# Kernel optimization log

Hardware: AMD Instinct MI355X
Metric: run time of the kernel (lower is better)

The kernel has to match this reference:

```python
import jax, jax.numpy as jnp
import numpy as np

B, S, E, H = 4, 2048, 1024, 16
K = 9           # number of boundaries per batch (K-1 = 8 passages)
DH = E // H


def make_relevance_mask(boundaries, relevance_scores, seq_len):
    """Vectorized equivalent of the Python-loop mask builder.

    boundaries: (B, K) int, sorted; boundaries[:,0] == q_end.
    relevance_scores: (B, K-1) float.
    Returns float mask (B, S, S) with values {0, 1, relevance}.
    """
    Bsz, Kb = boundaries.shape
    idx = jnp.arange(seq_len, dtype=boundaries.dtype)
    # pid[b, s] = j s.t. boundaries[b, j] <= s < boundaries[b, j+1]; -1 before b[0]
    pid = jax.vmap(lambda bb: jnp.searchsorted(bb, idx, side='right'))(boundaries) - 1  # (B,S)
    in_pass = (pid >= 0) & (pid < Kb - 1)  # inside some passage span
    rel_g = jnp.take_along_axis(relevance_scores, jnp.clip(pid, 0, Kb - 2), axis=1)  # (B,S)
    # query rows (pos < q_end): columns in passage j -> relevance[j], else 1
    col_val = jnp.where(in_pass, rel_g, 1.0)  # (B,S)
    qrow = idx[None, :] < boundaries[:, :1]   # (B,S)
    # non-query rows: 1 iff same passage block, else 0
    same = in_pass[:, :, None] & in_pass[:, None, :] & (pid[:, :, None] == pid[:, None, :])
    mask = jnp.where(qrow[:, :, None], col_val[:, None, :], jnp.where(same, 1.0, 0.0))
    return mask.astype(jnp.float32)


def setup_inputs() -> dict:
    key = jax.random.key(0)
    k1, k2, k3, k4, k5, k6, k7 = jax.random.split(key, 7)
    hidden_states = jax.random.normal(k1, (B, S, E), dtype=jnp.float32)
    relevance_scores = jax.random.uniform(k2, (B, K - 1), dtype=jnp.float32)
    passage_boundaries = jnp.sort(jax.random.randint(k3, (B, K), 0, S, dtype=jnp.int32), axis=1)
    in_proj_w = 0.02 * jax.random.normal(k4, (3 * E, E), dtype=jnp.float32)
    in_proj_b = jnp.zeros((3 * E,), dtype=jnp.float32)
    out_w = 0.02 * jax.random.normal(k5, (E, E), dtype=jnp.float32)
    out_b = jnp.zeros((E,), dtype=jnp.float32)
    return {
        'hidden_states': hidden_states,
        'relevance_scores': relevance_scores,
        'passage_boundaries': passage_boundaries,
        'in_proj_w': in_proj_w,
        'in_proj_b': in_proj_b,
        'out_w': out_w,
        'out_b': out_b,
    }


def reference(hidden_states, relevance_scores, passage_boundaries,
              in_proj_w, in_proj_b, out_w, out_b):
    Bsz, Sl, Em = hidden_states.shape
    mask = make_relevance_mask(passage_boundaries, relevance_scores, Sl)  # (B,S,S)
    qkv = hidden_states @ in_proj_w.T + in_proj_b              # (B,S,3E)
    q, k, v = jnp.split(qkv, 3, axis=-1)
    def heads(t):
        return t.reshape(Bsz, Sl, H, DH).transpose(0, 2, 1, 3)  # (B,H,S,Dh)
    q, k, v = heads(q), heads(k), heads(v)
    scale = 1.0 / jnp.sqrt(jnp.float32(DH))
    scores = jnp.einsum('bhqd,bhkd->bhqk', q * scale, k) + mask[:, None]  # float mask is ADDED
    attn = jax.nn.softmax(scores, axis=-1)
    out = jnp.einsum('bhqk,bhkd->bhqd', attn, v)
    out = out.transpose(0, 2, 1, 3).reshape(Bsz, Sl, Em)
    return out @ out_w.T + out_b
```

## Files before the change

### kernel.cpp

```cpp
#include <hip/hip_runtime.h>
#include <math.h>

#define Bsz 4
#define Sq  2048
#define Eq  1024
#define Hh  16
#define DHd 64
#define Kb  9
#define STR 72
#define GSTR 72

typedef _Float16 f16;
typedef __attribute__((ext_vector_type(8))) _Float16 fh8;
typedef __attribute__((ext_vector_type(4))) float fx4;

__global__ void pid_kernel(const int* __restrict__ bnd, const float* __restrict__ rel,
                           int* __restrict__ pidq, float* __restrict__ colval) {
  int idx = blockIdx.x * blockDim.x + threadIdx.x;
  if (idx >= Bsz * Sq) return;
  int b = idx >> 11;
  int s = idx & (Sq - 1);
  int j = -1;
#pragma unroll
  for (int t = 0; t < Kb; ++t) {
    if (bnd[b * Kb + t] <= s) j = t;
  }
  pidq[idx] = j;
  colval[idx] = (j >= 0 && j < Kb - 1) ? rel[b * (Kb - 1) + j] : 1.0f;
}

__global__ __launch_bounds__(256) void cvt_hs(const float* __restrict__ x,
                                              f16* __restrict__ xo) {
  int i = (blockIdx.x * blockDim.x + threadIdx.x) * 8;
  float4 a = *(const float4*)&x[i];
  float4 b = *(const float4*)&x[i + 4];
  fh8 o;
  o[0] = (f16)a.x; o[1] = (f16)a.y; o[2] = (f16)a.z; o[3] = (f16)a.w;
  o[4] = (f16)b.x; o[5] = (f16)b.y; o[6] = (f16)b.z; o[7] = (f16)b.w;
  *(fh8*)&xo[i] = o;
}

template <int MODE>
__global__ __launch_bounds__(256) void gemm_f16(
    const f16* __restrict__ A, const float* __restrict__ Bf,
    const float* __restrict__ bias, float* __restrict__ Cp,
    int M, int N, int Kd,
    f16* __restrict__ qo, f16* __restrict__ ko, f16* __restrict__ vto) {
  __shared__ __align__(16) f16 Ash[128 * GSTR];
  __shared__ __align__(16) f16 Bsh[128 * GSTR];

  const int tid = threadIdx.x;
  const int lane = tid & 63, w = tid >> 6;
  const int wm = w >> 1, wn = w & 1;
  const int q16 = lane & 15, quad = lane >> 4;
  const int m_blk = blockIdx.y * 128, n_blk = blockIdx.x * 128;

  fx4 acc[4][4];
#pragma unroll
  for (int mt = 0; mt < 4; ++mt)
#pragma unroll
    for (int nt = 0; nt < 4; ++nt)
#pragma unroll
      for (int r = 0; r < 4; ++r) acc[mt][nt][r] = 0.f;

  const int sr = tid >> 2, sc = (tid & 3) * 16;

  for (int k0 = 0; k0 < Kd; k0 += 64) {
    __syncthreads();
#pragma unroll
    for (int h = 0; h < 2; ++h) {
      const int r = sr + h * 64;
      const f16* ga = &A[(size_t)(m_blk + r) * Kd + k0 + sc];
      *(fh8*)&Ash[r * GSTR + sc]     = *(const fh8*)&ga[0];
      *(fh8*)&Ash[r * GSTR + sc + 8] = *(const fh8*)&ga[8];
      const float* gb = &Bf[(size_t)(n_blk + r) * Kd + k0 + sc];
      float4 f0 = *(const float4*)&gb[0];
      float4 f1 = *(const float4*)&gb[4];
      float4 f2 = *(const float4*)&gb[8];
      float4 f3 = *(const float4*)&gb[12];
      fh8 b0, b1;
      b0[0] = (f16)f0.x; b0[1] = (f16)f0.y; b0[2] = (f16)f0.z; b0[3] = (f16)f0.w;
      b0[4] = (f16)f1.x; b0[5] = (f16)f1.y; b0[6] = (f16)f1.z; b0[7] = (f16)f1.w;
      b1[0] = (f16)f2.x; b1[1] = (f16)f2.y; b1[2] = (f16)f2.z; b1[3] = (f16)f2.w;
      b1[4] = (f16)f3.x; b1[5] = (f16)f3.y; b1[6] = (f16)f3.z; b1[7] = (f16)f3.w;
      *(fh8*)&Bsh[r * GSTR + sc]     = b0;
      *(fh8*)&Bsh[r * GSTR + sc + 8] = b1;
    }
    __syncthreads();

#pragma unroll
    for (int ks = 0; ks < 2; ++ks) {
      fh8 af[4], bfr[4];
#pragma unroll
      for (int mt = 0; mt < 4; ++mt)
        af[mt] = *(const fh8*)&Ash[(wm * 64 + mt * 16 + q16) * GSTR + ks * 32 + quad * 8];
#pragma unroll
      for (int nt = 0; nt < 4; ++nt)
        bfr[nt] = *(const fh8*)&Bsh[(wn * 64 + nt * 16 + q16) * GSTR + ks * 32 + quad * 8];
#pragma unroll
      for (int nt = 0; nt < 4; ++nt)
#pragma unroll
        for (int mt = 0; mt < 4; ++mt)
          acc[mt][nt] = __builtin_amdgcn_mfma_f32_16x16x32_f16(af[mt], bfr[nt], acc[mt][nt], 0, 0, 0);
    }
  }

  float bsv[4];
#pragma unroll
  for (int nt = 0; nt < 4; ++nt) bsv[nt] = bias[n_blk + wn * 64 + nt * 16 + q16];

  if (MODE == 0) {
#pragma unroll
    for (int mt = 0; mt < 4; ++mt)
#pragma unroll
      for (int r = 0; r < 4; ++r) {
        int row = m_blk + wm * 64 + mt * 16 + quad * 4 + r;
#pragma unroll
        for (int nt = 0; nt < 4; ++nt) {
          int col = n_blk + wn * 64 + nt * 16 + q16;
          Cp[(size_t)row * N + col] = acc[mt][nt][r] + bsv[nt];
        }
      }
  } else {
    const int n0 = n_blk + wn * 64;
    const int which = n0 >> 10;
    const int hd = (n0 & 1023) >> 6;
    const float scale = (which == 0) ? 0.125f : 1.0f;
#pragma unroll
    for (int mt = 0; mt < 4; ++mt)
#pragma unroll
      for (int r = 0; r < 4; ++r) {
        int m = m_blk + wm * 64 + mt * 16 + quad * 4 + r;
        int b = m >> 11, s = m & (Sq - 1);
#pragma unroll
        for (int nt = 0; nt < 4; ++nt) {
          int d = nt * 16 + q16;
          float x = (acc[mt][nt][r] + bsv[nt]) * scale;
          if (which == 2) {
            vto[(((size_t)(b * Hh + hd)) * DHd + d) * Sq + s] = (f16)x;
          } else {
            f16* dst = (which == 0) ? qo : ko;
            dst[(((size_t)(b * Hh + hd)) * Sq + s) * DHd + d] = (f16)x;
          }
        }
      }
  }
}

__global__ __launch_bounds__(256, 3) void attn_f16(
    const f16* __restrict__ Qf, const f16* __restrict__ Kf,
    const f16* __restrict__ Vt, const int* __restrict__ pidq,
    const float* __restrict__ colval, f16* __restrict__ attf) {
  const int qb = blockIdx.x, hd = blockIdx.y, b = blockIdx.z;
  const int bh = b * Hh + hd;
  const int tid = threadIdx.x, lane = tid & 63, w = tid >> 6;
  const int q16 = lane & 15, quad = lane >> 4;

  __shared__ __align__(16) f16 Ks[64 * STR];
  __shared__ __align__(16) f16 Vs[64 * STR];
  __shared__ __align__(16) f16 Ps[4][32 * STR];

  const size_t qkbase = (size_t)bh * Sq * DHd;
  const size_t vtbase = (size_t)bh * DHd * Sq;

  fh8 qf[2][2];
#pragma unroll
  for (int mt = 0; mt < 2; ++mt)
#pragma unroll
    for (int ks = 0; ks < 2; ++ks)
      qf[mt][ks] = *(const fh8*)&Qf[qkbase +
          (size_t)(qb * 128 + w * 32 + mt * 16 + q16) * DHd + ks * 32 + quad * 8];

  int pq[8];
#pragma unroll
  for (int mt = 0; mt < 2; ++mt)
#pragma unroll
    for (int r = 0; r < 4; ++r)
      pq[mt * 4 + r] = pidq[b * Sq + qb * 128 + w * 32 + mt * 16 + quad * 4 + r];

  fh8 onesf;
#pragma unroll
  for (int j = 0; j < 8; ++j) onesf[j] = (q16 == 0) ? (f16)1.0f : (f16)0.0f;

  fx4 o_acc[2][4], lacc[2];
#pragma unroll
  for (int mt = 0; mt < 2; ++mt) {
#pragma unroll
    for (int r = 0; r < 4; ++r) lacc[mt][r] = 0.f;
#pragma unroll
    for (int dt = 0; dt < 4; ++dt)
#pragma unroll
      for (int r = 0; r < 4; ++r) o_acc[mt][dt][r] = 0.f;
  }

  for (int kt = 0; kt < 32; ++kt) {
    __syncthreads();
    {
      int n = tid >> 2, c = (tid & 3) * 16;
      size_t gk = qkbase + (size_t)(kt * 64 + n) * DHd + c;
      *(fh8*)&Ks[n * STR + c]     = *(const fh8*)&Kf[gk];
      *(fh8*)&Ks[n * STR + c + 8] = *(const fh8*)&Kf[gk + 8];
      size_t gv = vtbase + (size_t)n * Sq + kt * 64 + c;
      *(fh8*)&Vs[n * STR + c]     = *(const fh8*)&Vt[gv];
      *(fh8*)&Vs[n * STR + c + 8] = *(const fh8*)&Vt[gv + 8];
    }
    __syncthreads();

    fx4 sacc[2][4];
#pragma unroll
    for (int mt = 0; mt < 2; ++mt)
#pragma unroll
      for (int nt = 0; nt < 4; ++nt)
#pragma unroll
        for (int r = 0; r < 4; ++r) sacc[mt][nt][r] = 0.f;

#pragma unroll
    for (int ks = 0; ks < 2; ++ks)
#pragma unroll
      for (int nt = 0; nt < 4; ++nt) {
        fh8 kf8 = *(const fh8*)&Ks[(nt * 16 + q16) * STR + ks * 32 + quad * 8];
#pragma unroll
        for (int mt = 0; mt < 2; ++mt)
          sacc[mt][nt] = __builtin_amdgcn_mfma_f32_16x16x32_f16(qf[mt][ks], kf8, sacc[mt][nt], 0, 0, 0);
      }

    int pcm[4]; float cv[4];
#pragma unroll
    for (int nt = 0; nt < 4; ++nt) {
      int c = kt * 64 + nt * 16 + q16;
      int p = pidq[b * Sq + c];
      pcm[nt] = (p >= 0 && p < Kb - 1) ? p : -2;
      cv[nt] = colval[b * Sq + c];
    }

#pragma unroll
    for (int mt = 0; mt < 2; ++mt)
#pragma unroll
      for (int nt = 0; nt < 4; ++nt)
#pragma unroll
        for (int r = 0; r < 4; ++r) {
          int rq = pq[mt * 4 + r];
          float mv = (rq < 0) ? cv[nt] : ((rq == pcm[nt]) ? 1.0f : 0.0f);
          float p = __expf(sacc[mt][nt][r] + mv);
          Ps[w][(mt * 16 + quad * 4 + r) * STR + nt * 16 + q16] = (f16)p;
        }

#pragma unroll
    for (int ks2 = 0; ks2 < 2; ++ks2) {
      fh8 pf[2];
#pragma unroll
      for (int mt = 0; mt < 2; ++mt)
        pf[mt] = *(const fh8*)&Ps[w][(mt * 16 + q16) * STR + ks2 * 32 + quad * 8];
#pragma unroll
      for (int mt = 0; mt < 2; ++mt)
        lacc[mt] = __builtin_amdgcn_mfma_f32_16x16x32_f16(pf[mt], onesf, lacc[mt], 0, 0, 0);
#pragma unroll
      for (int dt = 0; dt < 4; ++dt) {
        fh8 vf = *(const fh8*)&Vs[(dt * 16 + q16) * STR + ks2 * 32 + quad * 8];
#pragma unroll
        for (int mt = 0; mt < 2; ++mt)
          o_acc[mt][dt] = __builtin_amdgcn_mfma_f32_16x16x32_f16(pf[mt], vf, o_acc[mt][dt], 0, 0, 0);
      }
    }
  }

#pragma unroll
  for (int mt = 0; mt < 2; ++mt)
#pragma unroll
    for (int r = 0; r < 4; ++r) {
      float l = __shfl(lacc[mt][r], (lane >> 4) << 4);
      float inv = 1.0f / l;
      int qg = qb * 128 + w * 32 + mt * 16 + quad * 4 + r;
      size_t base = ((size_t)(b * Sq + qg)) * Eq + hd * 64;
#pragma unroll
      for (int dt = 0; dt < 4; ++dt)
        attf[base + dt * 16 + q16] = (f16)(o_acc[mt][dt][r] * inv);
    }
}

extern "C" void kernel_launch(void* const* d_in, const int* in_sizes, int n_in,
                              void* d_out, int out_size, void* d_ws, size_t ws_size,
                              hipStream_t stream) {
  const float* hs = (const float*)d_in[0];
  const float* rel = (const float*)d_in[1];
  const int* bnd = (const int*)d_in[2];
  const float* wi = (const float*)d_in[3];
  const float* bi = (const float*)d_in[4];
  const float* wo = (const float*)d_in[5];
  const float* bo = (const float*)d_in[6];
  float* out = (float*)d_out;

  const size_t NQ = (size_t)Bsz * Hh * Sq * DHd;
  char* p = (char*)d_ws;
  f16* qf = (f16*)p;   p += NQ * 2;
  f16* kf = (f16*)p;   p += NQ * 2;
  f16* vt = (f16*)p;   p += NQ * 2;
  f16* hsf = (f16*)p;  p += NQ * 2;
  f16* attf = (f16*)p; p += NQ * 2;
  int* pidq = (int*)p; p += Bsz * Sq * 4;
  float* colv = (float*)p;

  hipLaunchKernelGGL(pid_kernel, dim3((Bsz * Sq + 255) / 256), dim3(256), 0, stream,
                     bnd, rel, pidq, colv);
  hipLaunchKernelGGL(cvt_hs, dim3((int)(NQ / 8 / 256)), dim3(256), 0, stream,
                     hs, hsf);
  hipLaunchKernelGGL((gemm_f16<1>), dim3(24, 64), dim3(256), 0, stream,
                     hsf, wi, bi, (float*)nullptr, Bsz * Sq, 3 * Eq, Eq,
                     qf, kf, vt);
  hipLaunchKernelGGL(attn_f16, dim3(16, 16, 4), dim3(256), 0, stream,
                     qf, kf, vt, pidq, colv, attf);
  hipLaunchKernelGGL((gemm_f16<0>), dim3(8, 64), dim3(256), 0, stream,
                     attf, wo, bo, out, Bsz * Sq, Eq, Eq,
                     nullptr, nullptr, nullptr);
}
```

Before: 355.2 us.

## Pre-convert weights to fp16, transpose score tiles, compute row sums in registers

Weights are converted to fp16 once per call in separate passes, so the GEMMs load fp16 B tiles directly instead of converting fp32 in every block. In attention, the QK^T MFMA operands are swapped so each lane holds one query row. Mask metadata can then be loaded as vector int4/float4 and the row sum accumulated in registers, which replaces the extra ones-vector MFMA. The exponent uses exp2 with a LOG2E prescale folded into colval. The trade-off is extra conversion launches and workspace memory.

```diff
diff --git a/kernel.cpp b/kernel.cpp
--- a/kernel.cpp
+++ b/kernel.cpp
@@ -8,9 +8,10 @@
 #define DHd 64
 #define Kb  9
 #define STR 72
-#define GSTR 72
+#define LOG2E 1.4426950408889634f
 
 typedef _Float16 f16;
+typedef __attribute__((ext_vector_type(2))) _Float16 fh2;
 typedef __attribute__((ext_vector_type(8))) _Float16 fh8;
 typedef __attribute__((ext_vector_type(4))) float fx4;
 
@@ -26,7 +27,7 @@
     if (bnd[b * Kb + t] <= s) j = t;
   }
   pidq[idx] = j;
-  colval[idx] = (j >= 0 && j < Kb - 1) ? rel[b * (Kb - 1) + j] : 1.0f;
+  colval[idx] = ((j >= 0 && j < Kb - 1) ? rel[b * (Kb - 1) + j] : 1.0f) * LOG2E;
 }
 
 __global__ __launch_bounds__(256) void cvt_hs(const float* __restrict__ x,
@@ -42,12 +43,12 @@
 
 template <int MODE>
 __global__ __launch_bounds__(256) void gemm_f16(
-    const f16* __restrict__ A, const float* __restrict__ Bf,
+    const f16* __restrict__ A, const f16* __restrict__ Bf,
     const float* __restrict__ bias, float* __restrict__ Cp,
     int M, int N, int Kd,
     f16* __restrict__ qo, f16* __restrict__ ko, f16* __restrict__ vto) {
-  __shared__ __align__(16) f16 Ash[128 * GSTR];
-  __shared__ __align__(16) f16 Bsh[128 * GSTR];
+  __shared__ __align__(16) f16 Ash[128 * STR];
+  __shared__ __align__(16) f16 Bsh[128 * STR];
 
   const int tid = threadIdx.x;
   const int lane = tid & 63, w = tid >> 6;
@@ -71,20 +72,11 @@
     for (int h = 0; h < 2; ++h) {
       const int r = sr + h * 64;
       const f16* ga = &A[(size_t)(m_blk + r) * Kd + k0 + sc];
-      *(fh8*)&Ash[r * GSTR + sc]     = *(const fh8*)&ga[0];
-      *(fh8*)&Ash[r * GSTR + sc + 8] = *(const fh8*)&ga[8];
-      const float* gb = &Bf[(size_t)(n_blk + r) * Kd + k0 + sc];
-      float4 f0 = *(const float4*)&gb[0];
-      float4 f1 = *(const float4*)&gb[4];
-      float4 f2 = *(const float4*)&gb[8];
-      float4 f3 = *(const float4*)&gb[12];
-      fh8 b0, b1;
-      b0[0] = (f16)f0.x; b0[1] = (f16)f0.y; b0[2] = (f16)f0.z; b0[3] = (f16)f0.w;
-      b0[4] = (f16)f1.x; b0[5] = (f16)f1.y; b0[6] = (f16)f1.z; b0[7] = (f16)f1.w;
-      b1[0] = (f16)f2.x; b1[1] = (f16)f2.y; b1[2] = (f16)f2.z; b1[3] = (f16)f2.w;
-      b1[4] = (f16)f3.x; b1[5] = (f16)f3.y; b1[6] = (f16)f3.z; b1[7] = (f16)f3.w;
-      *(fh8*)&Bsh[r * GSTR + sc]     = b0;
-      *(fh8*)&Bsh[r * GSTR + sc + 8] = b1;
+      *(fh8*)&Ash[r * STR + sc]     = *(const fh8*)&ga[0];
+      *(fh8*)&Ash[r * STR + sc + 8] = *(const fh8*)&ga[8];
+      const f16* gb = &Bf[(size_t)(n_blk + r) * Kd + k0 + sc];
+      *(fh8*)&Bsh[r * STR + sc]     = *(const fh8*)&gb[0];
+      *(fh8*)&Bsh[r * STR + sc + 8] = *(const fh8*)&gb[8];
     }
     __syncthreads();
 
@@ -93,10 +85,10 @@
       fh8 af[4], bfr[4];
 #pragma unroll
       for (int mt = 0; mt < 4; ++mt)
-        af[mt] = *(const fh8*)&Ash[(wm * 64 + mt * 16 + q16) * GSTR + ks * 32 + quad * 8];
+        af[mt] = *(const fh8*)&Ash[(wm * 64 + mt * 16 + q16) * STR + ks * 32 + quad * 8];
 #pragma unroll
       for (int nt = 0; nt < 4; ++nt)
-        bfr[nt] = *(const fh8*)&Bsh[(wn * 64 + nt * 16 + q16) * GSTR + ks * 32 + quad * 8];
+        bfr[nt] = *(const fh8*)&Bsh[(wn * 64 + nt * 16 + q16) * STR + ks * 32 + quad * 8];
 #pragma unroll
       for (int nt = 0; nt < 4; ++nt)
 #pragma unroll
@@ -171,27 +163,19 @@
       qf[mt][ks] = *(const fh8*)&Qf[qkbase +
           (size_t)(qb * 128 + w * 32 + mt * 16 + q16) * DHd + ks * 32 + quad * 8];
 
-  int pq[8];
+  int pqr[2];
 #pragma unroll
   for (int mt = 0; mt < 2; ++mt)
-#pragma unroll
-    for (int r = 0; r < 4; ++r)
-      pq[mt * 4 + r] = pidq[b * Sq + qb * 128 + w * 32 + mt * 16 + quad * 4 + r];
-
-  fh8 onesf;
-#pragma unroll
-  for (int j = 0; j < 8; ++j) onesf[j] = (q16 == 0) ? (f16)1.0f : (f16)0.0f;
-
-  fx4 o_acc[2][4], lacc[2];
-#pragma unroll
-  for (int mt = 0; mt < 2; ++mt) {
-#pragma unroll
-    for (int r = 0; r < 4; ++r) lacc[mt][r] = 0.f;
+    pqr[mt] = pidq[b * Sq + qb * 128 + w * 32 + mt * 16 + q16];
+
+  fx4 o_acc[2][4];
+  float lsum[2] = {0.f, 0.f};
+#pragma unroll
+  for (int mt = 0; mt < 2; ++mt)
 #pragma unroll
     for (int dt = 0; dt < 4; ++dt)
 #pragma unroll
       for (int r = 0; r < 4; ++r) o_acc[mt][dt][r] = 0.f;
-  }
 
   for (int kt = 0; kt < 32; ++kt) {
     __syncthreads();
@@ -206,44 +190,56 @@
     }
     __syncthreads();
 
-    fx4 sacc[2][4];
-#pragma unroll
-    for (int mt = 0; mt < 2; ++mt)
-#pragma unroll
-      for (int nt = 0; nt < 4; ++nt)
-#pragma unroll
-        for (int r = 0; r < 4; ++r) sacc[mt][nt][r] = 0.f;
+    fx4 sacc[4][2];
+#pragma unroll
+    for (int ct = 0; ct < 4; ++ct)
+#pragma unroll
+      for (int mt = 0; mt < 2; ++mt)
+#pragma unroll
+        for (int r = 0; r < 4; ++r) sacc[ct][mt][r] = 0.f;
 
 #pragma unroll
     for (int ks = 0; ks < 2; ++ks)
 #pragma unroll
-      for (int nt = 0; nt < 4; ++nt) {
-        fh8 kf8 = *(const fh8*)&Ks[(nt * 16 + q16) * STR + ks * 32 + quad * 8];
+      for (int ct = 0; ct < 4; ++ct) {
+        fh8 kf8 = *(const fh8*)&Ks[(ct * 16 + q16) * STR + ks * 32 + quad * 8];
 #pragma unroll
         for (int mt = 0; mt < 2; ++mt)
-          sacc[mt][nt] = __builtin_amdgcn_mfma_f32_16x16x32_f16(qf[mt][ks], kf8, sacc[mt][nt], 0, 0, 0);
-      }
-
-    int pcm[4]; float cv[4];
-#pragma unroll
-    for (int nt = 0; nt < 4; ++nt) {
-      int c = kt * 64 + nt * 16 + q16;
-      int p = pidq[b * Sq + c];
-      pcm[nt] = (p >= 0 && p < Kb - 1) ? p : -2;
-      cv[nt] = colval[b * Sq + c];
-    }
-
-#pragma unroll
-    for (int mt = 0; mt < 2; ++mt)
-#pragma unroll
-      for (int nt = 0; nt < 4; ++nt)
+          sacc[ct][mt] = __builtin_amdgcn_mfma_f32_16x16x32_f16(kf8, qf[mt][ks], sacc[ct][mt], 0, 0, 0);
+      }
+
+    int4 p4[4]; float4 c4[4];
+#pragma unroll
+    for (int ct = 0; ct < 4; ++ct) {
+      int c0 = kt * 64 + ct * 16 + quad * 4;
+      p4[ct] = *(const int4*)&pidq[b * Sq + c0];
+      c4[ct] = *(const float4*)&colval[b * Sq + c0];
+    }
+
+#pragma unroll
+    for (int mt = 0; mt < 2; ++mt) {
+      const int rq = pqr[mt];
+      const bool isq = rq < 0;
+      const int prow = (mt * 16 + q16) * STR;
+#pragma unroll
+      for (int ct = 0; ct < 4; ++ct) {
+        float pr[4];
+        const int pv[4] = {p4[ct].x, p4[ct].y, p4[ct].z, p4[ct].w};
+        const float cl[4] = {c4[ct].x, c4[ct].y, c4[ct].z, c4[ct].w};
 #pragma unroll
         for (int r = 0; r < 4; ++r) {
-          int rq = pq[mt * 4 + r];
-          float mv = (rq < 0) ? cv[nt] : ((rq == pcm[nt]) ? 1.0f : 0.0f);
-          float p = __expf(sacc[mt][nt][r] + mv);
-          Ps[w][(mt * 16 + quad * 4 + r) * STR + nt * 16 + q16] = (f16)p;
+          int pc = ((unsigned)pv[r] < 8u) ? pv[r] : -2;
+          float mvl2 = isq ? cl[r] : ((rq == pc) ? LOG2E : 0.f);
+          pr[r] = exp2f(fmaf(sacc[ct][mt][r], LOG2E, mvl2));
         }
+        lsum[mt] += (pr[0] + pr[1]) + (pr[2] + pr[3]);
+        fh2 pk0, pk1;
+        pk0[0] = (f16)pr[0]; pk0[1] = (f16)pr[1];
+        pk1[0] = (f16)pr[2]; pk1[1] = (f16)pr[3];
+        *(fh2*)&Ps[w][prow + ct * 16 + quad * 4]     = pk0;
+        *(fh2*)&Ps[w][prow + ct * 16 + quad * 4 + 2] = pk1;
+      }
+    }
 
 #pragma unroll
     for (int ks2 = 0; ks2 < 2; ++ks2) {
@@ -252,9 +248,6 @@
       for (int mt = 0; mt < 2; ++mt)
         pf[mt] = *(const fh8*)&Ps[w][(mt * 16 + q16) * STR + ks2 * 32 + quad * 8];
 #pragma unroll
-      for (int mt = 0; mt < 2; ++mt)
-        lacc[mt] = __builtin_amdgcn_mfma_f32_16x16x32_f16(pf[mt], onesf, lacc[mt], 0, 0, 0);
-#pragma unroll
       for (int dt = 0; dt < 4; ++dt) {
         fh8 vf = *(const fh8*)&Vs[(dt * 16 + q16) * STR + ks2 * 32 + quad * 8];
 #pragma unroll
@@ -265,17 +258,21 @@
   }
 
 #pragma unroll
-  for (int mt = 0; mt < 2; ++mt)
+  for (int mt = 0; mt < 2; ++mt) {
+    float l = lsum[mt];
+    l += __shfl_xor(l, 16);
+    l += __shfl_xor(l, 32);
+    float inv = 1.0f / l;
 #pragma unroll
     for (int r = 0; r < 4; ++r) {
-      float l = __shfl(lacc[mt][r], (lane >> 4) << 4);
-      float inv = 1.0f / l;
+      float invr = __shfl(inv, quad * 4 + r);
       int qg = qb * 128 + w * 32 + mt * 16 + quad * 4 + r;
       size_t base = ((size_t)(b * Sq + qg)) * Eq + hd * 64;
 #pragma unroll
       for (int dt = 0; dt < 4; ++dt)
-        attf[base + dt * 16 + q16] = (f16)(o_acc[mt][dt][r] * inv);
-    }
+        attf[base + dt * 16 + q16] = (f16)(o_acc[mt][dt][r] * invr);
+    }
+  }
 }
 
 extern "C" void kernel_launch(void* const* d_in, const int* in_sizes, int n_in,
@@ -291,25 +288,30 @@
   float* out = (float*)d_out;
 
   const size_t NQ = (size_t)Bsz * Hh * Sq * DHd;
+  const size_t NWI = (size_t)3 * Eq * Eq;
+  const size_t NWO = (size_t)Eq * Eq;
   char* p = (char*)d_ws;
   f16* qf = (f16*)p;   p += NQ * 2;
   f16* kf = (f16*)p;   p += NQ * 2;
   f16* vt = (f16*)p;   p += NQ * 2;
   f16* hsf = (f16*)p;  p += NQ * 2;
   f16* attf = (f16*)p; p += NQ * 2;
+  f16* wif = (f16*)p;  p += NWI * 2;
+  f16* wof = (f16*)p;  p += NWO * 2;
   int* pidq = (int*)p; p += Bsz * Sq * 4;
   float* colv = (float*)p;
 
   hipLaunchKernelGGL(pid_kernel, dim3((Bsz * Sq + 255) / 256), dim3(256), 0, stream,
                      bnd, rel, pidq, colv);
-  hipLaunchKernelGGL(cvt_hs, dim3((int)(NQ / 8 / 256)), dim3(256), 0, stream,
-                     hs, hsf);
+  hipLaunchKernelGGL(cvt_hs, dim3((int)(NQ / 2048)), dim3(256), 0, stream, hs, hsf);
+  hipLaunchKernelGGL(cvt_hs, dim3((int)(NWI / 2048)), dim3(256), 0, stream, wi, wif);
+  hipLaunchKernelGGL(cvt_hs, dim3((int)(NWO / 2048)), dim3(256), 0, stream, wo, wof);
   hipLaunchKernelGGL((gemm_f16<1>), dim3(24, 64), dim3(256), 0, stream,
-                     hsf, wi, bi, (float*)nullptr, Bsz * Sq, 3 * Eq, Eq,
+                     hsf, wif, bi, (float*)nullptr, Bsz * Sq, 3 * Eq, Eq,
                      qf, kf, vt);
   hipLaunchKernelGGL(attn_f16, dim3(16, 16, 4), dim3(256), 0, stream,
                      qf, kf, vt, pidq, colv, attf);
   hipLaunchKernelGGL((gemm_f16<0>), dim3(8, 64), dim3(256), 0, stream,
-                     attf, wo, bo, out, Bsz * Sq, Eq, Eq,
+                     attf, wof, bo, out, Bsz * Sq, Eq, Eq,
                      nullptr, nullptr, nullptr);
 }
```

Measured after the change: 377.3 us. 6.2% more time.
